# Optimization experiments

Hardware: AMD Instinct MI355X
Metric: run time of the kernel (lower is better)

Reference implementation:

```python
import jax, jax.numpy as jnp
import numpy as np

N, E = 50000, 800000
IN, HID, OUT, T = 96, 128, 64, 8
THETA = 0.5


def setup_inputs() -> dict:
    key = jax.random.key(0)
    ks = jax.random.split(key, 8)
    x = jax.random.normal(ks[0], (N, IN), dtype=jnp.float32)
    edge_weight = jax.random.uniform(ks[1], (E,), dtype=jnp.float32)
    W1 = jax.random.normal(ks[2], (IN, HID), dtype=jnp.float32) * (2.0 / np.sqrt(IN + HID))
    W2 = jax.random.normal(ks[3], (HID, OUT), dtype=jnp.float32) * (2.0 / np.sqrt(HID + OUT))
    # Bernoulli(1 - theta) masks, fixed per MC sample (created in __init__)
    mask1 = (jax.random.uniform(ks[4], (T, IN, HID)) < (1.0 - THETA)).astype(jnp.float32)
    mask2 = (jax.random.uniform(ks[5], (T, HID, OUT)) < (1.0 - THETA)).astype(jnp.float32)
    src = jax.random.randint(ks[6], (E,), 0, N, dtype=jnp.int32)
    dst = jax.random.randint(ks[7], (E,), 0, N, dtype=jnp.int32)
    return {"x": x, "edge_weight": edge_weight, "W1": W1, "W2": W2,
            "mask1": mask1, "mask2": mask2, "src": src, "dst": dst}


def _spmm(feat, edge_weight, src, dst, n_nodes):
    # u_mul_e('feat','edge_weight') followed by fn.sum onto dst nodes
    msg = feat[src] * edge_weight[:, None]          # [E, D]
    return jax.ops.segment_sum(msg, dst, num_segments=n_nodes)  # [N, D]


def reference(x, edge_weight, W1, W2, mask1, mask2, src, dst):
    n = x.shape[0]
    # first aggregation is mask-independent -> compute once, share across T samples
    agg1 = _spmm(x, edge_weight, src, dst, n)       # [N, IN]

    def per_sample(m1, m2):
        h = jax.nn.relu(agg1 @ (W1 * m1))           # [N, HID]
        agg2 = _spmm(h, edge_weight, src, dst, n)   # [N, HID]
        return agg2 @ (W2 * m2)                     # [N, OUT]

    # stack of the T per-sample outputs (torch version returns a list)
    return jax.vmap(per_sample)(mask1, mask2)       # [T, N, OUT]
```

## Files before the change

### kernel.cpp

```cpp
#include <hip/hip_runtime.h>

#define N_NODES 50000
#define N_EDGES 800000
#define IN_F 96
#define HID_F 128
#define OUT_F 64
#define T_S 8
#define SCAN_B 196

typedef __attribute__((ext_vector_type(8))) short short8;
typedef __attribute__((ext_vector_type(4))) float float4v;

__device__ __forceinline__ float bf2f(unsigned short h) {
    unsigned u = ((unsigned)h) << 16;
    float f;
    __builtin_memcpy(&f, &u, 4);
    return f;
}
__device__ __forceinline__ unsigned short f2bf(float f) {
    unsigned u;
    __builtin_memcpy(&u, &f, 4);
    unsigned r = (u + 0x7fffu + ((u >> 16) & 1u)) >> 16;
    return (unsigned short)r;
}
__device__ __forceinline__ float bf_lo(unsigned u) {
    unsigned v = u << 16;
    float f;
    __builtin_memcpy(&f, &v, 4);
    return f;
}
__device__ __forceinline__ float bf_hi(unsigned u) {
    unsigned v = u & 0xffff0000u;
    float f;
    __builtin_memcpy(&f, &v, 4);
    return f;
}

__global__ void k_count(const int* __restrict__ dst, int* __restrict__ cnt) {
    int e = blockIdx.x * 256 + threadIdx.x;
    if (e < N_EDGES) atomicAdd(&cnt[dst[e]], 1);
}

__global__ __launch_bounds__(256) void k_scan1(const int* __restrict__ cnt,
                                               int* __restrict__ excl,
                                               int* __restrict__ blockSums) {
    __shared__ int buf[256];
    int tid = threadIdx.x;
    int idx = blockIdx.x * 256 + tid;
    int v = (idx < N_NODES) ? cnt[idx] : 0;
    buf[tid] = v;
    __syncthreads();
    for (int off = 1; off < 256; off <<= 1) {
        int t = buf[tid];
        int u = (tid >= off) ? buf[tid - off] : 0;
        __syncthreads();
        buf[tid] = t + u;
        __syncthreads();
    }
    int incl = buf[tid];
    if (idx < N_NODES) excl[idx] = incl - v;
    if (tid == 255) blockSums[blockIdx.x] = incl;
}

__global__ __launch_bounds__(256) void k_scan2(const int* __restrict__ blockSums,
                                               int* __restrict__ blockOff) {
    __shared__ int buf[256];
    int tid = threadIdx.x;
    int v = (tid < SCAN_B) ? blockSums[tid] : 0;
    buf[tid] = v;
    __syncthreads();
    for (int off = 1; off < 256; off <<= 1) {
        int t = buf[tid];
        int u = (tid >= off) ? buf[tid - off] : 0;
        __syncthreads();
        buf[tid] = t + u;
        __syncthreads();
    }
    if (tid < SCAN_B) blockOff[tid] = buf[tid] - v;
}

__global__ __launch_bounds__(256) void k_scan3(const int* __restrict__ excl,
                                               const int* __restrict__ blockOff,
                                               int* __restrict__ row_ptr,
                                               int* __restrict__ cursor) {
    int idx = blockIdx.x * 256 + threadIdx.x;
    if (idx < N_NODES) {
        int p = excl[idx] + blockOff[blockIdx.x];
        row_ptr[idx] = p;
        cursor[idx] = p;
    }
    if (idx == 0) row_ptr[N_NODES] = N_EDGES;
}

__global__ void k_fill(const int* __restrict__ src, const int* __restrict__ dst,
                       const float* __restrict__ ew, int* __restrict__ cursor,
                       int* __restrict__ csr_src, float* __restrict__ csr_w) {
    int e = blockIdx.x * 256 + threadIdx.x;
    if (e < N_EDGES) {
        int d = dst[e];
        int pos = atomicAdd(&cursor[d], 1);
        csr_src[pos] = src[e];
        csr_w[pos] = ew[e];
    }
}

__global__ void k_xb(const float* __restrict__ x, unsigned short* __restrict__ xb) {
    int i = blockIdx.x * 256 + threadIdx.x;
    int idx = i * 4;
    if (idx < N_NODES * IN_F) {
        float4 v = *(const float4*)(x + idx);
        uint2 r;
        r.x = (unsigned)f2bf(v.x) | ((unsigned)f2bf(v.y) << 16);
        r.y = (unsigned)f2bf(v.z) | ((unsigned)f2bf(v.w) << 16);
        *(uint2*)(xb + idx) = r;
    }
}

__global__ __launch_bounds__(256) void k_spmm1(const unsigned short* __restrict__ xb,
                                               const int* __restrict__ row_ptr,
                                               const int* __restrict__ csr_src,
                                               const float* __restrict__ csr_w,
                                               unsigned short* __restrict__ agg1) {
    int wave = threadIdx.x >> 6, lane = threadIdx.x & 63;
    int node = blockIdx.x * 4 + wave;
    if (lane >= 48) return;
    int beg = row_ptr[node], end = row_ptr[node + 1];
    const unsigned* xrow = (const unsigned*)xb;
    float a0 = 0.f, a1 = 0.f;
    int e = beg;
    for (; e + 7 < end; e += 8) {
        int s[8];
        float wv[8];
        unsigned d[8];
#pragma unroll
        for (int i = 0; i < 8; i++) {
            s[i] = csr_src[e + i];
            wv[i] = csr_w[e + i];
        }
#pragma unroll
        for (int i = 0; i < 8; i++) d[i] = xrow[(size_t)s[i] * 48 + lane];
#pragma unroll
        for (int i = 0; i < 8; i++) {
            a0 = fmaf(wv[i], bf_lo(d[i]), a0);
            a1 = fmaf(wv[i], bf_hi(d[i]), a1);
        }
    }
    for (; e < end; e++) {
        int s = csr_src[e];
        float wv = csr_w[e];
        unsigned d = xrow[(size_t)s * 48 + lane];
        a0 = fmaf(wv, bf_lo(d), a0);
        a1 = fmaf(wv, bf_hi(d), a1);
    }
    ((unsigned*)agg1)[(size_t)node * 48 + lane] =
        (unsigned)f2bf(a0) | ((unsigned)f2bf(a1) << 16);
}

__global__ void k_wprep(const float* __restrict__ W1, const float* __restrict__ W2,
                        const float* __restrict__ m1, const float* __restrict__ m2,
                        unsigned short* __restrict__ wf) {
    int gid = blockIdx.x * 256 + threadIdx.x;
    if (gid >= T_S * 20480) return;
    int t = gid / 20480;
    int idx = gid % 20480;
    float val;
    if (idx < 12288) {
        int j = idx & 7, lane = (idx >> 3) & 63, fr = idx >> 9;
        int kk = fr >> 3, nt = fr & 7;
        int k = kk * 32 + (lane >> 4) * 8 + j;
        int n = nt * 16 + (lane & 15);
        val = W1[k * HID_F + n] * m1[((size_t)t * IN_F + k) * HID_F + n];
    } else {
        int i2 = idx - 12288;
        int j = i2 & 7, lane = (i2 >> 3) & 63, fr = i2 >> 9;
        int kk = fr >> 2, ot = fr & 3;
        int k = kk * 32 + (lane >> 4) * 8 + j;
        int o = ot * 16 + (lane & 15);
        val = W2[k * OUT_F + o] * m2[((size_t)t * HID_F + k) * OUT_F + o];
    }
    wf[gid] = f2bf(val);
}

__global__ __launch_bounds__(256) void k_gemm(const unsigned short* __restrict__ agg1,
                                              const unsigned short* __restrict__ wfrags,
                                              unsigned short* __restrict__ P, int tBase,
                                              int nodeStride, int tMul) {
    __shared__ __align__(16) unsigned short ldsW[20480];
    __shared__ __align__(16) unsigned short ldsH[4][2176];
    int t = tBase + blockIdx.y;
    const uint4* wsrc = (const uint4*)(wfrags + (size_t)t * 20480);
    uint4* wdst = (uint4*)ldsW;
    for (int i = threadIdx.x; i < 2560; i += 256) wdst[i] = wsrc[i];
    __syncthreads();

    int wave = threadIdx.x >> 6, lane = threadIdx.x & 63;
    int quad = lane >> 4, l15 = lane & 15;
    int node = blockIdx.x * 64 + wave * 16 + l15;
    bool v = node < N_NODES;

    short8 a[3];
    if (v) {
        const unsigned short* ap = agg1 + (size_t)node * IN_F;
        a[0] = *(const short8*)(ap + 0 * 32 + quad * 8);
        a[1] = *(const short8*)(ap + 1 * 32 + quad * 8);
        a[2] = *(const short8*)(ap + 2 * 32 + quad * 8);
    } else {
        short8 z = {0, 0, 0, 0, 0, 0, 0, 0};
        a[0] = z; a[1] = z; a[2] = z;
    }

    for (int nt = 0; nt < 8; nt++) {
        float4v acc = {0.f, 0.f, 0.f, 0.f};
        for (int kk = 0; kk < 3; kk++) {
            short8 w = *(const short8*)&ldsW[(kk * 8 + nt) * 512 + lane * 8];
            acc = __builtin_amdgcn_mfma_f32_16x16x32_bf16(w, a[kk], acc, 0, 0, 0);
        }
        unsigned h0 = f2bf(fmaxf(acc[0], 0.f));
        unsigned h1 = f2bf(fmaxf(acc[1], 0.f));
        unsigned h2 = f2bf(fmaxf(acc[2], 0.f));
        unsigned h3 = f2bf(fmaxf(acc[3], 0.f));
        uint2 pk;
        pk.x = h0 | (h1 << 16);
        pk.y = h2 | (h3 << 16);
        *(uint2*)&ldsH[wave][l15 * 136 + nt * 16 + quad * 4] = pk;
    }

    short8 hf[4];
    for (int kk = 0; kk < 4; kk++)
        hf[kk] = *(const short8*)&ldsH[wave][l15 * 136 + kk * 32 + quad * 8];

    unsigned short* Pt = P + (size_t)node * nodeStride + (size_t)t * tMul;
    for (int ot = 0; ot < 4; ot++) {
        float4v acc = {0.f, 0.f, 0.f, 0.f};
        for (int kk = 0; kk < 4; kk++) {
            short8 w = *(const short8*)&ldsW[12288 + (kk * 4 + ot) * 512 + lane * 8];
            acc = __builtin_amdgcn_mfma_f32_16x16x32_bf16(w, hf[kk], acc, 0, 0, 0);
        }
        if (v) {
            uint2 pk;
            pk.x = (unsigned)f2bf(acc[0]) | ((unsigned)f2bf(acc[1]) << 16);
            pk.y = (unsigned)f2bf(acc[2]) | ((unsigned)f2bf(acc[3]) << 16);
            *(uint2*)(Pt + ot * 16 + quad * 4) = pk;
        }
    }
}

__global__ __launch_bounds__(256) void k_spmm2(const unsigned short* __restrict__ P,
                                               const int* __restrict__ row_ptr,
                                               const int* __restrict__ csr_src,
                                               const float* __restrict__ csr_w,
                                               float* __restrict__ out) {
    int wave = threadIdx.x >> 6, lane = threadIdx.x & 63;
    int node = blockIdx.x * 4 + wave;
    int beg = row_ptr[node], end = row_ptr[node + 1];
    const uint4* Pl = (const uint4*)P + lane;
    float acc[8] = {0.f, 0.f, 0.f, 0.f, 0.f, 0.f, 0.f, 0.f};
    int e = beg;
    for (; e + 7 < end; e += 8) {
        int s[8];
        float wv[8];
        uint4 d[8];
#pragma unroll
        for (int i = 0; i < 8; i++) {
            s[i] = csr_src[e + i];
            wv[i] = csr_w[e + i];
        }
#pragma unroll
        for (int i = 0; i < 8; i++) d[i] = Pl[(size_t)s[i] * 64];
#pragma unroll
        for (int i = 0; i < 8; i++) {
            acc[0] = fmaf(wv[i], bf_lo(d[i].x), acc[0]);
            acc[1] = fmaf(wv[i], bf_hi(d[i].x), acc[1]);
            acc[2] = fmaf(wv[i], bf_lo(d[i].y), acc[2]);
            acc[3] = fmaf(wv[i], bf_hi(d[i].y), acc[3]);
            acc[4] = fmaf(wv[i], bf_lo(d[i].z), acc[4]);
            acc[5] = fmaf(wv[i], bf_hi(d[i].z), acc[5]);
            acc[6] = fmaf(wv[i], bf_lo(d[i].w), acc[6]);
            acc[7] = fmaf(wv[i], bf_hi(d[i].w), acc[7]);
        }
    }
    for (; e < end; e++) {
        int s = csr_src[e];
        float wv = csr_w[e];
        uint4 d = Pl[(size_t)s * 64];
        acc[0] = fmaf(wv, bf_lo(d.x), acc[0]);
        acc[1] = fmaf(wv, bf_hi(d.x), acc[1]);
        acc[2] = fmaf(wv, bf_lo(d.y), acc[2]);
        acc[3] = fmaf(wv, bf_hi(d.y), acc[3]);
        acc[4] = fmaf(wv, bf_lo(d.z), acc[4]);
        acc[5] = fmaf(wv, bf_hi(d.z), acc[5]);
        acc[6] = fmaf(wv, bf_lo(d.w), acc[6]);
        acc[7] = fmaf(wv, bf_hi(d.w), acc[7]);
    }
    int t = lane >> 3, o = (lane & 7) * 8;
    float* op = out + ((size_t)t * N_NODES + node) * OUT_F + o;
    float4 v0 = {acc[0], acc[1], acc[2], acc[3]};
    float4 v1 = {acc[4], acc[5], acc[6], acc[7]};
    *(float4*)op = v0;
    *(float4*)(op + 4) = v1;
}

__global__ __launch_bounds__(512) void k_spmm2_1t(const unsigned short* __restrict__ P,
                                                  const int* __restrict__ row_ptr,
                                                  const int* __restrict__ csr_src,
                                                  const float* __restrict__ csr_w,
                                                  float* __restrict__ out) {
    int node = blockIdx.x * 8 + (threadIdx.x >> 6);
    int o = threadIdx.x & 63;
    if (node >= N_NODES) return;
    int beg = row_ptr[node], end = row_ptr[node + 1];
    const unsigned short* Pt = P + o;
    float a0 = 0.f, a1 = 0.f, a2 = 0.f, a3 = 0.f;
    int e = beg;
    for (; e + 3 < end; e += 4) {
        int s0 = csr_src[e], s1 = csr_src[e + 1], s2 = csr_src[e + 2], s3 = csr_src[e + 3];
        float w0 = csr_w[e], w1 = csr_w[e + 1], w2 = csr_w[e + 2], w3 = csr_w[e + 3];
        a0 += w0 * bf2f(Pt[(size_t)s0 * OUT_F]);
        a1 += w1 * bf2f(Pt[(size_t)s1 * OUT_F]);
        a2 += w2 * bf2f(Pt[(size_t)s2 * OUT_F]);
        a3 += w3 * bf2f(Pt[(size_t)s3 * OUT_F]);
    }
    for (; e < end; e++) a0 += csr_w[e] * bf2f(Pt[(size_t)csr_src[e] * OUT_F]);
    out[(size_t)node * OUT_F + o] = a0 + a1 + a2 + a3;
}

extern "C" void kernel_launch(void* const* d_in, const int* in_sizes, int n_in,
                              void* d_out, int out_size, void* d_ws, size_t ws_size,
                              hipStream_t stream) {
    const float* x = (const float*)d_in[0];
    const float* ew = (const float*)d_in[1];
    const float* W1 = (const float*)d_in[2];
    const float* W2 = (const float*)d_in[3];
    const float* m1 = (const float*)d_in[4];
    const float* m2 = (const float*)d_in[5];
    const int* src = (const int*)d_in[6];
    const int* dst = (const int*)d_in[7];
    float* out = (float*)d_out;

    char* w = (char*)d_ws;
    size_t off = 0;
    auto alloc = [&](size_t bytes) -> void* {
        void* p = (void*)(w + off);
        off += (bytes + 255) & ~(size_t)255;
        return p;
    };
    int* cnt = (int*)alloc((size_t)N_NODES * 4);
    int* row_ptr = (int*)alloc((size_t)(N_NODES + 1) * 4);
    int* cursor = (int*)alloc((size_t)N_NODES * 4);
    int* excl = (int*)alloc((size_t)N_NODES * 4);
    int* blockSums = (int*)alloc((size_t)SCAN_B * 4);
    int* blockOff = (int*)alloc((size_t)SCAN_B * 4);
    int* csr_src = (int*)alloc((size_t)N_EDGES * 4);
    float* csr_w = (float*)alloc((size_t)N_EDGES * 4);
    unsigned short* agg1 = (unsigned short*)alloc((size_t)N_NODES * IN_F * 2);
    unsigned short* wf = (unsigned short*)alloc((size_t)T_S * 20480 * 2);

    size_t unionBase = off;
    size_t pBytesBatched = (size_t)T_S * N_NODES * OUT_F * 2;
    size_t xbBytes = (size_t)N_NODES * IN_F * 2;
    bool batched = ws_size >= unionBase + (pBytesBatched > xbBytes ? pBytesBatched : xbBytes);
    unsigned short* xb = (unsigned short*)(w + unionBase);
    unsigned short* P = (unsigned short*)(w + unionBase);
    if (!batched) {
        xb = (unsigned short*)(w + unionBase);
        P = (unsigned short*)(w + unionBase + ((xbBytes + 255) & ~(size_t)255));
    }

    hipMemsetAsync(cnt, 0, (size_t)N_NODES * 4, stream);
    k_count<<<N_EDGES / 256, 256, 0, stream>>>(dst, cnt);
    k_scan1<<<SCAN_B, 256, 0, stream>>>(cnt, excl, blockSums);
    k_scan2<<<1, 256, 0, stream>>>(blockSums, blockOff);
    k_scan3<<<SCAN_B, 256, 0, stream>>>(excl, blockOff, row_ptr, cursor);
    k_fill<<<N_EDGES / 256, 256, 0, stream>>>(src, dst, ew, cursor, csr_src, csr_w);
    k_xb<<<(N_NODES * IN_F / 4 + 255) / 256, 256, 0, stream>>>(x, xb);
    k_spmm1<<<N_NODES / 4, 256, 0, stream>>>(xb, row_ptr, csr_src, csr_w, agg1);
    k_wprep<<<(T_S * 20480) / 256, 256, 0, stream>>>(W1, W2, m1, m2, wf);

    if (batched) {
        k_gemm<<<dim3(782, 8), 256, 0, stream>>>(agg1, wf, P, 0, T_S * OUT_F, OUT_F);
        k_spmm2<<<N_NODES / 4, 256, 0, stream>>>(P, row_ptr, csr_src, csr_w, out);
    } else {
        for (int t = 0; t < T_S; t++) {
            k_gemm<<<dim3(782, 1), 256, 0, stream>>>(agg1, wf, P, t, OUT_F, 0);
            k_spmm2_1t<<<6250, 512, 0, stream>>>(P, row_ptr, csr_src, csr_w,
                                                 out + (size_t)t * N_NODES * OUT_F);
        }
    }
}
```

Measured before the change: 432.6 us.

## Fuse prep kernels, branchless padded SpMM loops, add nontemporal loads/stores

Merges the degree count, x-to-bf16 conversion and weight-fragment prep into one launch, cutting two kernel launches and letting the independent work run concurrently. The SpMM loops drop their scalar tails in favour of clamped, zero-weighted padded batches, with spmm1 widened to 16 edges per batch for more memory-level parallelism. CSR reads and the P and output writes use nontemporal hints. xb and P now get separate workspace regions instead of aliasing, which raises the workspace needed to take the batched path.

```diff
diff --git a/kernel.cpp b/kernel.cpp
--- a/kernel.cpp
+++ b/kernel.cpp
@@ -10,6 +10,8 @@
 
 typedef __attribute__((ext_vector_type(8))) short short8;
 typedef __attribute__((ext_vector_type(4))) float float4v;
+typedef __attribute__((ext_vector_type(2))) unsigned int uint2v;
+typedef __attribute__((ext_vector_type(4))) unsigned int uint4v;
 
 __device__ __forceinline__ float bf2f(unsigned short h) {
     unsigned u = ((unsigned)h) << 16;
@@ -36,9 +38,50 @@
     return f;
 }
 
-__global__ void k_count(const int* __restrict__ dst, int* __restrict__ cnt) {
-    int e = blockIdx.x * 256 + threadIdx.x;
-    if (e < N_EDGES) atomicAdd(&cnt[dst[e]], 1);
+__global__ __launch_bounds__(256) void k_prep(const int* __restrict__ dst,
+                                              int* __restrict__ cnt,
+                                              const float* __restrict__ x,
+                                              unsigned short* __restrict__ xb,
+                                              const float* __restrict__ W1,
+                                              const float* __restrict__ W2,
+                                              const float* __restrict__ m1,
+                                              const float* __restrict__ m2,
+                                              unsigned short* __restrict__ wf) {
+    int b = blockIdx.x;
+    if (b < 3125) {
+        int e = b * 256 + threadIdx.x;
+        atomicAdd(&cnt[dst[e]], 1);
+    } else if (b < 7813) {
+        int i = (b - 3125) * 256 + threadIdx.x;
+        int idx = i * 4;
+        if (idx < N_NODES * IN_F) {
+            float4 v = *(const float4*)(x + idx);
+            uint2v r;
+            r.x = (unsigned)f2bf(v.x) | ((unsigned)f2bf(v.y) << 16);
+            r.y = (unsigned)f2bf(v.z) | ((unsigned)f2bf(v.w) << 16);
+            *(uint2v*)(xb + idx) = r;
+        }
+    } else {
+        int gid = (b - 7813) * 256 + threadIdx.x;
+        int t = gid / 20480;
+        int idx = gid % 20480;
+        float val;
+        if (idx < 12288) {
+            int j = idx & 7, lane = (idx >> 3) & 63, fr = idx >> 9;
+            int kk = fr >> 3, nt = fr & 7;
+            int k = kk * 32 + (lane >> 4) * 8 + j;
+            int n = nt * 16 + (lane & 15);
+            val = W1[k * HID_F + n] * m1[((size_t)t * IN_F + k) * HID_F + n];
+        } else {
+            int i2 = idx - 12288;
+            int j = i2 & 7, lane = (i2 >> 3) & 63, fr = i2 >> 9;
+            int kk = fr >> 2, ot = fr & 3;
+            int k = kk * 32 + (lane >> 4) * 8 + j;
+            int o = ot * 16 + (lane & 15);
+            val = W2[k * OUT_F + o] * m2[((size_t)t * HID_F + k) * OUT_F + o];
+        }
+        wf[gid] = f2bf(val);
+    }
 }
 
 __global__ __launch_bounds__(256) void k_scan1(const int* __restrict__ cnt,
@@ -104,18 +147,6 @@
     }
 }
 
-__global__ void k_xb(const float* __restrict__ x, unsigned short* __restrict__ xb) {
-    int i = blockIdx.x * 256 + threadIdx.x;
-    int idx = i * 4;
-    if (idx < N_NODES * IN_F) {
-        float4 v = *(const float4*)(x + idx);
-        uint2 r;
-        r.x = (unsigned)f2bf(v.x) | ((unsigned)f2bf(v.y) << 16);
-        r.y = (unsigned)f2bf(v.z) | ((unsigned)f2bf(v.w) << 16);
-        *(uint2*)(xb + idx) = r;
-    }
-}
-
 __global__ __launch_bounds__(256) void k_spmm1(const unsigned short* __restrict__ xb,
                                                const int* __restrict__ row_ptr,
                                                const int* __restrict__ csr_src,
@@ -125,60 +156,31 @@
     int node = blockIdx.x * 4 + wave;
     if (lane >= 48) return;
     int beg = row_ptr[node], end = row_ptr[node + 1];
+    int last = end - 1;
     const unsigned* xrow = (const unsigned*)xb;
     float a0 = 0.f, a1 = 0.f;
-    int e = beg;
-    for (; e + 7 < end; e += 8) {
-        int s[8];
-        float wv[8];
-        unsigned d[8];
-#pragma unroll
-        for (int i = 0; i < 8; i++) {
-            s[i] = csr_src[e + i];
-            wv[i] = csr_w[e + i];
-        }
-#pragma unroll
-        for (int i = 0; i < 8; i++) d[i] = xrow[(size_t)s[i] * 48 + lane];
-#pragma unroll
-        for (int i = 0; i < 8; i++) {
+    for (int e = beg; e < end; e += 16) {
+        int s[16];
+        float wv[16];
+        unsigned d[16];
+#pragma unroll
+        for (int i = 0; i < 16; i++) {
+            int ee = e + i;
+            int ii = (ee < end) ? ee : last;
+            s[i] = __builtin_nontemporal_load(&csr_src[ii]);
+            float wl = __builtin_nontemporal_load(&csr_w[ii]);
+            wv[i] = (ee < end) ? wl : 0.f;
+        }
+#pragma unroll
+        for (int i = 0; i < 16; i++) d[i] = xrow[(size_t)s[i] * 48 + lane];
+#pragma unroll
+        for (int i = 0; i < 16; i++) {
             a0 = fmaf(wv[i], bf_lo(d[i]), a0);
             a1 = fmaf(wv[i], bf_hi(d[i]), a1);
         }
     }
-    for (; e < end; e++) {
-        int s = csr_src[e];
-        float wv = csr_w[e];
-        unsigned d = xrow[(size_t)s * 48 + lane];
-        a0 = fmaf(wv, bf_lo(d), a0);
-        a1 = fmaf(wv, bf_hi(d), a1);
-    }
     ((unsigned*)agg1)[(size_t)node * 48 + lane] =
         (unsigned)f2bf(a0) | ((unsigned)f2bf(a1) << 16);
-}
-
-__global__ void k_wprep(const float* __restrict__ W1, const float* __restrict__ W2,
-                        const float* __restrict__ m1, const float* __restrict__ m2,
-                        unsigned short* __restrict__ wf) {
-    int gid = blockIdx.x * 256 + threadIdx.x;
-    if (gid >= T_S * 20480) return;
-    int t = gid / 20480;
-    int idx = gid % 20480;
-    float val;
-    if (idx < 12288) {
-        int j = idx & 7, lane = (idx >> 3) & 63, fr = idx >> 9;
-        int kk = fr >> 3, nt = fr & 7;
-        int k = kk * 32 + (lane >> 4) * 8 + j;
-        int n = nt * 16 + (lane & 15);
-        val = W1[k * HID_F + n] * m1[((size_t)t * IN_F + k) * HID_F + n];
-    } else {
-        int i2 = idx - 12288;
-        int j = i2 & 7, lane = (i2 >> 3) & 63, fr = i2 >> 9;
-        int kk = fr >> 2, ot = fr & 3;
-        int k = kk * 32 + (lane >> 4) * 8 + j;
-        int o = ot * 16 + (lane & 15);
-        val = W2[k * OUT_F + o] * m2[((size_t)t * HID_F + k) * OUT_F + o];
-    }
-    wf[gid] = f2bf(val);
 }
 
 __global__ __launch_bounds__(256) void k_gemm(const unsigned short* __restrict__ agg1,
@@ -188,8 +190,8 @@
     __shared__ __align__(16) unsigned short ldsW[20480];
     __shared__ __align__(16) unsigned short ldsH[4][2176];
     int t = tBase + blockIdx.y;
-    const uint4* wsrc = (const uint4*)(wfrags + (size_t)t * 20480);
-    uint4* wdst = (uint4*)ldsW;
+    const uint4v* wsrc = (const uint4v*)(wfrags + (size_t)t * 20480);
+    uint4v* wdst = (uint4v*)ldsW;
     for (int i = threadIdx.x; i < 2560; i += 256) wdst[i] = wsrc[i];
     __syncthreads();
 
@@ -219,10 +221,10 @@
         unsigned h1 = f2bf(fmaxf(acc[1], 0.f));
         unsigned h2 = f2bf(fmaxf(acc[2], 0.f));
         unsigned h3 = f2bf(fmaxf(acc[3], 0.f));
-        uint2 pk;
+        uint2v pk;
         pk.x = h0 | (h1 << 16);
         pk.y = h2 | (h3 << 16);
-        *(uint2*)&ldsH[wave][l15 * 136 + nt * 16 + quad * 4] = pk;
+        *(uint2v*)&ldsH[wave][l15 * 136 + nt * 16 + quad * 4] = pk;
     }
 
     short8 hf[4];
@@ -237,10 +239,10 @@
             acc = __builtin_amdgcn_mfma_f32_16x16x32_bf16(w, hf[kk], acc, 0, 0, 0);
         }
         if (v) {
-            uint2 pk;
+            uint2v pk;
             pk.x = (unsigned)f2bf(acc[0]) | ((unsigned)f2bf(acc[1]) << 16);
             pk.y = (unsigned)f2bf(acc[2]) | ((unsigned)f2bf(acc[3]) << 16);
-            *(uint2*)(Pt + ot * 16 + quad * 4) = pk;
+            __builtin_nontemporal_store(pk, (uint2v*)(Pt + ot * 16 + quad * 4));
         }
     }
 }
@@ -253,17 +255,20 @@
     int wave = threadIdx.x >> 6, lane = threadIdx.x & 63;
     int node = blockIdx.x * 4 + wave;
     int beg = row_ptr[node], end = row_ptr[node + 1];
-    const uint4* Pl = (const uint4*)P + lane;
+    int last = end - 1;
+    const uint4v* Pl = (const uint4v*)P + lane;
     float acc[8] = {0.f, 0.f, 0.f, 0.f, 0.f, 0.f, 0.f, 0.f};
-    int e = beg;
-    for (; e + 7 < end; e += 8) {
+    for (int e = beg; e < end; e += 8) {
         int s[8];
         float wv[8];
-        uint4 d[8];
+        uint4v d[8];
 #pragma unroll
         for (int i = 0; i < 8; i++) {
-            s[i] = csr_src[e + i];
-            wv[i] = csr_w[e + i];
+            int ee = e + i;
+            int ii = (ee < end) ? ee : last;
+            s[i] = __builtin_nontemporal_load(&csr_src[ii]);
+            float wl = __builtin_nontemporal_load(&csr_w[ii]);
+            wv[i] = (ee < end) ? wl : 0.f;
         }
 #pragma unroll
         for (int i = 0; i < 8; i++) d[i] = Pl[(size_t)s[i] * 64];
@@ -279,25 +284,12 @@
             acc[7] = fmaf(wv[i], bf_hi(d[i].w), acc[7]);
         }
     }
-    for (; e < end; e++) {
-        int s = csr_src[e];
-        float wv = csr_w[e];
-        uint4 d = Pl[(size_t)s * 64];
-        acc[0] = fmaf(wv, bf_lo(d.x), acc[0]);
-        acc[1] = fmaf(wv, bf_hi(d.x), acc[1]);
-        acc[2] = fmaf(wv, bf_lo(d.y), acc[2]);
-        acc[3] = fmaf(wv, bf_hi(d.y), acc[3]);
-        acc[4] = fmaf(wv, bf_lo(d.z), acc[4]);
-        acc[5] = fmaf(wv, bf_hi(d.z), acc[5]);
-        acc[6] = fmaf(wv, bf_lo(d.w), acc[6]);
-        acc[7] = fmaf(wv, bf_hi(d.w), acc[7]);
-    }
     int t = lane >> 3, o = (lane & 7) * 8;
     float* op = out + ((size_t)t * N_NODES + node) * OUT_F + o;
-    float4 v0 = {acc[0], acc[1], acc[2], acc[3]};
-    float4 v1 = {acc[4], acc[5], acc[6], acc[7]};
-    *(float4*)op = v0;
-    *(float4*)(op + 4) = v1;
+    float4v v0 = {acc[0], acc[1], acc[2], acc[3]};
+    float4v v1 = {acc[4], acc[5], acc[6], acc[7]};
+    __builtin_nontemporal_store(v0, (float4v*)op);
+    __builtin_nontemporal_store(v1, (float4v*)(op + 4));
 }
 
 __global__ __launch_bounds__(512) void k_spmm2_1t(const unsigned short* __restrict__ P,
@@ -355,26 +347,20 @@
     unsigned short* agg1 = (unsigned short*)alloc((size_t)N_NODES * IN_F * 2);
     unsigned short* wf = (unsigned short*)alloc((size_t)T_S * 20480 * 2);
 
-    size_t unionBase = off;
+    size_t xbBytes = (size_t)N_NODES * IN_F * 2;
     size_t pBytesBatched = (size_t)T_S * N_NODES * OUT_F * 2;
-    size_t xbBytes = (size_t)N_NODES * IN_F * 2;
-    bool batched = ws_size >= unionBase + (pBytesBatched > xbBytes ? pBytesBatched : xbBytes);
-    unsigned short* xb = (unsigned short*)(w + unionBase);
-    unsigned short* P = (unsigned short*)(w + unionBase);
-    if (!batched) {
-        xb = (unsigned short*)(w + unionBase);
-        P = (unsigned short*)(w + unionBase + ((xbBytes + 255) & ~(size_t)255));
-    }
+    unsigned short* xb = (unsigned short*)alloc(xbBytes);
+    bool batched = ws_size >= off + pBytesBatched;
+    unsigned short* P = (unsigned short*)alloc(batched ? pBytesBatched
+                                                       : (size_t)N_NODES * OUT_F * 2);
 
     hipMemsetAsync(cnt, 0, (size_t)N_NODES * 4, stream);
-    k_count<<<N_EDGES / 256, 256, 0, stream>>>(dst, cnt);
+    k_prep<<<8453, 256, 0, stream>>>(dst, cnt, x, xb, W1, W2, m1, m2, wf);
     k_scan1<<<SCAN_B, 256, 0, stream>>>(cnt, excl, blockSums);
     k_scan2<<<1, 256, 0, stream>>>(blockSums, blockOff);
     k_scan3<<<SCAN_B, 256, 0, stream>>>(excl, blockOff, row_ptr, cursor);
     k_fill<<<N_EDGES / 256, 256, 0, stream>>>(src, dst, ew, cursor, csr_src, csr_w);
-    k_xb<<<(N_NODES * IN_F / 4 + 255) / 256, 256, 0, stream>>>(x, xb);
     k_spmm1<<<N_NODES / 4, 256, 0, stream>>>(xb, row_ptr, csr_src, csr_w, agg1);
-    k_wprep<<<(T_S * 20480) / 256, 256, 0, stream>>>(W1, W2, m1, m2, wf);
 
     if (batched) {
         k_gemm<<<dim3(782, 8), 256, 0, stream>>>(agg1, wf, P, 0, T_S * OUT_F, OUT_F);
```

Result: slower. 442.1 us (+2.2%).
